# Kernel tuning notes

Hardware: AMD Instinct MI355X
Metric: run time of the kernel (lower is better)

## Reference

```python
import jax, jax.numpy as jnp
import numpy as np

B, V, H, T, D, HD = 4, 384, 128, 16, 8, 64
N = V + H  # 512
relu = jax.nn.relu


def setup_inputs() -> dict:
    key = jax.random.key(0)
    ks = jax.random.split(key, 12)

    def w(k, i, o):
        return (jax.random.normal(k, (i, o), jnp.float32) / np.sqrt(i)).astype(jnp.float32)

    return {
        "x": jax.random.normal(ks[0], (B, V, T, D), jnp.float32),
        "adj": jax.random.uniform(ks[1], (B, N, N), jnp.float32),
        # input_proj: Linear(T*D, HD) -> ReLU -> Linear(HD, HD) -> ReLU
        "w_in1": w(ks[2], T * D, HD), "b_in1": jnp.zeros((HD,), jnp.float32),
        "w_in2": w(ks[3], HD, HD), "b_in2": jnp.zeros((HD,), jnp.float32),
        # edge_mlp: Linear(2*HD, HD) -> ReLU -> Linear(HD, HD) -> ReLU
        "w_e1": w(ks[4], 2 * HD, HD), "b_e1": jnp.zeros((HD,), jnp.float32),
        "w_e2": w(ks[5], HD, HD), "b_e2": jnp.zeros((HD,), jnp.float32),
        # node_mlp: Linear(HD, HD) -> ReLU -> Linear(HD, HD) -> ReLU
        "w_n1": w(ks[6], HD, HD), "b_n1": jnp.zeros((HD,), jnp.float32),
        "w_n2": w(ks[7], HD, HD), "b_n2": jnp.zeros((HD,), jnp.float32),
        # out_proj: Linear(HD, T*D)
        "w_out": w(ks[8], HD, T * D), "b_out": jnp.zeros((T * D,), jnp.float32),
    }


def reference(x, adj, w_in1, b_in1, w_in2, b_in2, w_e1, b_e1, w_e2, b_e2,
              w_n1, b_n1, w_n2, b_n2, w_out, b_out):
    # node embedding of visible nodes: (B,V,HD)
    h = relu(relu(x.reshape(B, V, T * D) @ w_in1 + b_in1) @ w_in2 + b_in2)
    # pad hidden nodes with zeros: (B,N,HD)
    h_full = jnp.zeros((B, N, HD), x.dtype).at[:, :V].set(h)
    # edge_mlp layer 1 on cat([h_i, h_j]): split weight instead of materializing
    # the (B,N,N,2*HD) concatenation — same math.
    a = h_full @ w_e1[:HD]   # receiver-side contribution (B,N,HD)
    b = h_full @ w_e1[HD:]   # sender-side contribution  (B,N,HD)
    e = relu(a[:, :, None, :] + b[:, None, :, :] + b_e1)   # (B,N,N,HD)
    e = relu(e @ w_e2 + b_e2)                               # (B,N,N,HD)
    # mask by adjacency and sum over senders j
    agg = jnp.einsum('bijh,bij->bih', e, adj)               # (B,N,HD)
    n = relu(relu(agg @ w_n1 + b_n1) @ w_n2 + b_n2)         # (B,N,HD)
    out = n[:, V:] @ w_out + b_out                          # (B,H,T*D)
    return out.reshape(B, H, T, D)
```

## Files before the change

kernel.cpp:

```cpp
#include <hip/hip_runtime.h>

#define BQ 4
#define VV 384
#define HH 128
#define NN 512
#define HDIM 64
#define TD 128

typedef float f32x2 __attribute__((ext_vector_type(2)));

__device__ __forceinline__ float BCAST(float v, int l) {
    return __int_as_float(__builtin_amdgcn_readlane(__float_as_int(v), l));
}
__device__ __forceinline__ f32x2 RELU2(f32x2 v) {
    f32x2 r; r.x = fmaxf(v.x, 0.f); r.y = fmaxf(v.y, 0.f); return r;
}

__global__ __launch_bounds__(512) void k_rowpipe(
    const float* __restrict__ x,
    const float* __restrict__ w_in1,
    const float* __restrict__ b_in1,
    const float* __restrict__ w_in2,
    const float* __restrict__ b_in2,
    const float* __restrict__ w_e1,
    const float* __restrict__ b_e1,
    const float* __restrict__ w_e2,
    const float* __restrict__ b_e2,
    float* __restrict__ E2)
{
    __shared__ f32x2 part[4][8][HDIM];

    const int o    = threadIdx.x >> 6;
    const int lane = threadIdx.x & 63;
    const int row0 = blockIdx.x * 2;

    const float* xr0 = x + (size_t)row0 * TD;
    const float* xr1 = xr0 + TD;
    const float xv = (lane < 32) ? xr0[16 * o + (lane & 15)]
                                 : xr1[16 * o + (lane & 15)];

    f32x2 a0 = {0.f, 0.f}, a1 = {0.f, 0.f};
    #pragma unroll
    for (int k = 0; k < 16; k += 2) {
        const int kg = 16 * o + k;
        f32x2 s0; s0.x = BCAST(xv, k);     s0.y = BCAST(xv, 32 + k);
        f32x2 s1; s1.x = BCAST(xv, k + 1); s1.y = BCAST(xv, 33 + k);
        a0 += s0 * w_in1[kg * HDIM + lane];
        a1 += s1 * w_in1[(kg + 1) * HDIM + lane];
    }
    part[0][o][lane] = a0 + a1;
    __syncthreads();
    f32x2 t = ((part[0][0][lane] + part[0][1][lane])
             + (part[0][2][lane] + part[0][3][lane]))
            + ((part[0][4][lane] + part[0][5][lane])
             + (part[0][6][lane] + part[0][7][lane]));
    const f32x2 h1 = RELU2(t + b_in1[lane]);
    const float h1x = h1.x, h1y = h1.y;

    a0 = (f32x2){0.f, 0.f}; a1 = (f32x2){0.f, 0.f};
    #pragma unroll
    for (int k = 0; k < 8; k += 2) {
        const int kg = 8 * o + k;
        f32x2 s0; s0.x = BCAST(h1x, kg);     s0.y = BCAST(h1y, kg);
        f32x2 s1; s1.x = BCAST(h1x, kg + 1); s1.y = BCAST(h1y, kg + 1);
        a0 += s0 * w_in2[kg * HDIM + lane];
        a1 += s1 * w_in2[(kg + 1) * HDIM + lane];
    }
    part[1][o][lane] = a0 + a1;
    __syncthreads();
    t = ((part[1][0][lane] + part[1][1][lane])
       + (part[1][2][lane] + part[1][3][lane]))
      + ((part[1][4][lane] + part[1][5][lane])
       + (part[1][6][lane] + part[1][7][lane]));
    const f32x2 h2 = RELU2(t + b_in2[lane]);
    const float h2x = h2.x, h2y = h2.y;

    a0 = (f32x2){0.f, 0.f}; a1 = (f32x2){0.f, 0.f};
    #pragma unroll
    for (int k = 0; k < 8; k += 2) {
        const int kg = 8 * o + k;
        f32x2 s0; s0.x = BCAST(h2x, kg);     s0.y = BCAST(h2y, kg);
        f32x2 s1; s1.x = BCAST(h2x, kg + 1); s1.y = BCAST(h2y, kg + 1);
        a0 += s0 * w_e1[(HDIM + kg) * HDIM + lane];
        a1 += s1 * w_e1[(HDIM + kg + 1) * HDIM + lane];
    }
    part[2][o][lane] = a0 + a1;
    __syncthreads();
    t = ((part[2][0][lane] + part[2][1][lane])
       + (part[2][2][lane] + part[2][3][lane]))
      + ((part[2][4][lane] + part[2][5][lane])
       + (part[2][6][lane] + part[2][7][lane]));
    const f32x2 e1 = RELU2(t + b_e1[lane]);
    const float e1x = e1.x, e1y = e1.y;

    a0 = (f32x2){0.f, 0.f}; a1 = (f32x2){0.f, 0.f};
    #pragma unroll
    for (int k = 0; k < 8; k += 2) {
        const int kg = 8 * o + k;
        f32x2 s0; s0.x = BCAST(e1x, kg);     s0.y = BCAST(e1y, kg);
        f32x2 s1; s1.x = BCAST(e1x, kg + 1); s1.y = BCAST(e1y, kg + 1);
        a0 += s0 * w_e2[kg * HDIM + lane];
        a1 += s1 * w_e2[(kg + 1) * HDIM + lane];
    }
    part[3][o][lane] = a0 + a1;
    __syncthreads();
    if (o == 0) {
        t = ((part[3][0][lane] + part[3][1][lane])
           + (part[3][2][lane] + part[3][3][lane]))
          + ((part[3][4][lane] + part[3][5][lane])
           + (part[3][6][lane] + part[3][7][lane]));
        const f32x2 e2v = RELU2(t + b_e2[lane]);
        E2[(size_t)row0 * HDIM + lane]       = e2v.x;
        E2[(size_t)(row0 + 1) * HDIM + lane] = e2v.y;
    }
}

__global__ __launch_bounds__(1024) void k_agg_out(
    const float* __restrict__ adj,
    const float* __restrict__ E2,
    const float* __restrict__ b_e1, const float* __restrict__ w_e2,
    const float* __restrict__ b_e2,
    const float* __restrict__ w_n1, const float* __restrict__ b_n1,
    const float* __restrict__ w_n2, const float* __restrict__ b_n2,
    const float* __restrict__ w_out,
    const float* __restrict__ b_out,
    float* __restrict__ out)
{
    const int blk  = blockIdx.x;
    const int b    = blk >> 6;
    const int pair = blk & 63;
    const int wid  = threadIdx.x >> 6;
    const int lane = threadIdx.x & 63;

    const int i0 = VV + pair * 2;
    const float* adjr0 = adj + ((size_t)b * NN + i0) * NN;
    const float* adjr1 = adjr0 + NN;
    const int j0 = wid * 32;

    const float adjv = (lane < 32) ? adjr0[j0 + lane] : adjr1[j0 + lane - 32];

    __shared__ float redA[12][2][HDIM];
    __shared__ float hs[4][2];
    __shared__ float e2c[HDIM];

    if (wid < 12) {
        const float* e2b = E2 + ((size_t)b * VV + j0) * HDIM;
        float p0 = 0.f, p1 = 0.f, q0 = 0.f, q1 = 0.f;
        #pragma unroll 8
        for (int jj = 0; jj < 32; jj += 2) {
            const float e0 = e2b[jj * HDIM + lane];
            const float e1 = e2b[(jj + 1) * HDIM + lane];
            p0 = fmaf(BCAST(adjv, jj),      e0, p0);
            q0 = fmaf(BCAST(adjv, 32 + jj), e0, q0);
            p1 = fmaf(BCAST(adjv, jj + 1),  e1, p1);
            q1 = fmaf(BCAST(adjv, 33 + jj), e1, q1);
        }
        redA[wid][0][lane] = p0 + p1;
        redA[wid][1][lane] = q0 + q1;
    } else {
        float s = adjv;
        s += __shfl_xor(s, 1, 64);
        s += __shfl_xor(s, 2, 64);
        s += __shfl_xor(s, 4, 64);
        s += __shfl_xor(s, 8, 64);
        s += __shfl_xor(s, 16, 64);
        if (lane == 0)  hs[wid - 12][0] = s;
        if (lane == 32) hs[wid - 12][1] = s;
        if (wid == 12) {
            const float e1c = fmaxf(b_e1[lane], 0.f);
            float t0 = b_e2[lane], t1 = 0.f;
            #pragma unroll 8
            for (int k = 0; k < HDIM; k += 2) {
                t0 = fmaf(BCAST(e1c, k),     w_e2[k * HDIM + lane],       t0);
                t1 = fmaf(BCAST(e1c, k + 1), w_e2[(k + 1) * HDIM + lane], t1);
            }
            e2c[lane] = fmaxf(t0 + t1, 0.f);
        }
    }
    __syncthreads();

    const int g  = wid >> 3;
    const int w8 = wid & 7;

    const float hsum = hs[0][g] + hs[1][g] + hs[2][g] + hs[3][g];
    float agg = hsum * e2c[lane];
    #pragma unroll
    for (int w = 0; w < 12; ++w) agg += redA[w][g][lane];

    __shared__ float redB[16][HDIM];
    {
        float t0 = 0.f, t1 = 0.f;
        #pragma unroll
        for (int t = 0; t < 8; t += 2) {
            const int k = 8 * w8 + t;
            t0 = fmaf(BCAST(agg, k),     w_n1[k * HDIM + lane],       t0);
            t1 = fmaf(BCAST(agg, k + 1), w_n1[(k + 1) * HDIM + lane], t1);
        }
        redB[wid][lane] = t0 + t1;
    }
    __syncthreads();
    float n1 = b_n1[lane];
    #pragma unroll
    for (int w = 0; w < 8; ++w) n1 += redB[g * 8 + w][lane];
    n1 = fmaxf(n1, 0.f);

    __shared__ float redC[16][HDIM];
    {
        float t0 = 0.f, t1 = 0.f;
        #pragma unroll
        for (int t = 0; t < 8; t += 2) {
            const int k = 8 * w8 + t;
            t0 = fmaf(BCAST(n1, k),     w_n2[k * HDIM + lane],       t0);
            t1 = fmaf(BCAST(n1, k + 1), w_n2[(k + 1) * HDIM + lane], t1);
        }
        redC[wid][lane] = t0 + t1;
    }
    __syncthreads();
    float n2 = b_n2[lane];
    #pragma unroll
    for (int w = 0; w < 8; ++w) n2 += redC[g * 8 + w][lane];
    n2 = fmaxf(n2, 0.f);

    __shared__ float redD[16][TD];
    {
        float o0 = 0.f, o1 = 0.f;
        #pragma unroll
        for (int t = 0; t < 8; ++t) {
            const int k = 8 * w8 + t;
            const float v = BCAST(n2, k);
            o0 = fmaf(v, w_out[k * TD + lane],      o0);
            o1 = fmaf(v, w_out[k * TD + 64 + lane], o1);
        }
        redD[wid][lane]      = o0;
        redD[wid][64 + lane] = o1;
    }
    __syncthreads();

    if (w8 < 2) {
        const int col = w8 * 64 + lane;
        float o = b_out[col];
        #pragma unroll
        for (int w = 0; w < 8; ++w) o += redD[g * 8 + w][col];
        const int orow = b * HH + pair * 2 + g;
        out[(size_t)orow * TD + col] = o;
    }
}

extern "C" void kernel_launch(void* const* d_in, const int* in_sizes, int n_in,
                              void* d_out, int out_size, void* d_ws, size_t ws_size,
                              hipStream_t stream) {
    const float* x     = (const float*)d_in[0];
    const float* adj   = (const float*)d_in[1];
    const float* w_in1 = (const float*)d_in[2];
    const float* b_in1 = (const float*)d_in[3];
    const float* w_in2 = (const float*)d_in[4];
    const float* b_in2 = (const float*)d_in[5];
    const float* w_e1  = (const float*)d_in[6];
    const float* b_e1  = (const float*)d_in[7];
    const float* w_e2  = (const float*)d_in[8];
    const float* b_e2  = (const float*)d_in[9];
    const float* w_n1  = (const float*)d_in[10];
    const float* b_n1  = (const float*)d_in[11];
    const float* w_n2  = (const float*)d_in[12];
    const float* b_n2  = (const float*)d_in[13];
    const float* w_out = (const float*)d_in[14];
    const float* b_out = (const float*)d_in[15];
    float* out = (float*)d_out;
    float* E2  = (float*)d_ws;

    k_rowpipe<<<BQ * VV / 2, 512, 0, stream>>>(
        x, w_in1, b_in1, w_in2, b_in2, w_e1, b_e1, w_e2, b_e2, E2);
    k_agg_out<<<BQ * HH / 2, 1024, 0, stream>>>(
        adj, E2, b_e1, w_e2, b_e2, w_n1, b_n1, w_n2, b_n2, w_out, b_out, out);
}
```

Before: 16.04 us.

## Move hidden-sender adjacency sums and constant edge vector into first kernel

Adds a ninth wave to the row-pipeline kernel that computes, for each hidden receiver row, the adjacency sum over hidden senders, plus the constant edge-MLP output for zero-embedding nodes. Both are written to workspace. The aggregation kernel can then spread all 16 waves over the 384 visible senders (24 each) instead of keeping 4 waves mostly idle. This aims to cut the critical path of the second kernel. In exchange, the first kernel runs larger blocks whose extra wave just matches the __syncthreads calls, and the second kernel does extra global reads.

```diff
diff --git a/kernel.cpp b/kernel.cpp
--- a/kernel.cpp
+++ b/kernel.cpp
@@ -16,8 +16,13 @@
     f32x2 r; r.x = fmaxf(v.x, 0.f); r.y = fmaxf(v.y, 0.f); return r;
 }
 
-__global__ __launch_bounds__(512) void k_rowpipe(
+#define OFF_E2   0
+#define OFF_HSUM (BQ * VV * HDIM)
+#define OFF_E2C  (OFF_HSUM + BQ * HH)
+
+__global__ __launch_bounds__(576) void k_rowpipe(
     const float* __restrict__ x,
+    const float* __restrict__ adj,
     const float* __restrict__ w_in1,
     const float* __restrict__ b_in1,
     const float* __restrict__ w_in2,
@@ -26,12 +31,44 @@
     const float* __restrict__ b_e1,
     const float* __restrict__ w_e2,
     const float* __restrict__ b_e2,
-    float* __restrict__ E2)
+    float* __restrict__ E2,
+    float* __restrict__ hsumW,
+    float* __restrict__ e2cW)
 {
     __shared__ f32x2 part[4][8][HDIM];
 
-    const int o    = threadIdx.x >> 6;
+    const int wid  = threadIdx.x >> 6;
     const int lane = threadIdx.x & 63;
+
+    if (wid == 8) {
+        if (blockIdx.x < BQ * HH) {
+            const int hr = blockIdx.x;
+            const int b  = hr >> 7;
+            const int hi = hr & 127;
+            const float* ar = adj + ((size_t)b * NN + VV + hi) * NN + VV;
+            float s = ar[lane] + ar[64 + lane];
+            s += __shfl_xor(s, 32, 64);
+            s += __shfl_xor(s, 16, 64);
+            s += __shfl_xor(s, 8, 64);
+            s += __shfl_xor(s, 4, 64);
+            s += __shfl_xor(s, 2, 64);
+            s += __shfl_xor(s, 1, 64);
+            if (lane == 0) hsumW[hr] = s;
+        } else if (blockIdx.x == BQ * HH) {
+            const float e1c = fmaxf(b_e1[lane], 0.f);
+            float t0 = b_e2[lane], t1 = 0.f;
+            #pragma unroll 8
+            for (int k = 0; k < HDIM; k += 2) {
+                t0 = fmaf(BCAST(e1c, k),     w_e2[k * HDIM + lane],       t0);
+                t1 = fmaf(BCAST(e1c, k + 1), w_e2[(k + 1) * HDIM + lane], t1);
+            }
+            e2cW[lane] = fmaxf(t0 + t1, 0.f);
+        }
+        __syncthreads(); __syncthreads(); __syncthreads(); __syncthreads();
+        return;
+    }
+
+    const int o    = wid;
     const int row0 = blockIdx.x * 2;
 
     const float* xr0 = x + (size_t)row0 * TD;
@@ -118,8 +155,8 @@
 __global__ __launch_bounds__(1024) void k_agg_out(
     const float* __restrict__ adj,
     const float* __restrict__ E2,
-    const float* __restrict__ b_e1, const float* __restrict__ w_e2,
-    const float* __restrict__ b_e2,
+    const float* __restrict__ hsumW,
+    const float* __restrict__ e2cW,
     const float* __restrict__ w_n1, const float* __restrict__ b_n1,
     const float* __restrict__ w_n2, const float* __restrict__ b_n2,
     const float* __restrict__ w_out,
@@ -135,19 +172,17 @@
     const int i0 = VV + pair * 2;
     const float* adjr0 = adj + ((size_t)b * NN + i0) * NN;
     const float* adjr1 = adjr0 + NN;
-    const int j0 = wid * 32;
+    const int j0 = wid * 24;
 
     const float adjv = (lane < 32) ? adjr0[j0 + lane] : adjr1[j0 + lane - 32];
 
-    __shared__ float redA[12][2][HDIM];
-    __shared__ float hs[4][2];
-    __shared__ float e2c[HDIM];
-
-    if (wid < 12) {
+    __shared__ float redA[16][2][HDIM];
+
+    {
         const float* e2b = E2 + ((size_t)b * VV + j0) * HDIM;
         float p0 = 0.f, p1 = 0.f, q0 = 0.f, q1 = 0.f;
-        #pragma unroll 8
-        for (int jj = 0; jj < 32; jj += 2) {
+        #pragma unroll
+        for (int jj = 0; jj < 24; jj += 2) {
             const float e0 = e2b[jj * HDIM + lane];
             const float e1 = e2b[(jj + 1) * HDIM + lane];
             p0 = fmaf(BCAST(adjv, jj),      e0, p0);
@@ -157,35 +192,16 @@
         }
         redA[wid][0][lane] = p0 + p1;
         redA[wid][1][lane] = q0 + q1;
-    } else {
-        float s = adjv;
-        s += __shfl_xor(s, 1, 64);
-        s += __shfl_xor(s, 2, 64);
-        s += __shfl_xor(s, 4, 64);
-        s += __shfl_xor(s, 8, 64);
-        s += __shfl_xor(s, 16, 64);
-        if (lane == 0)  hs[wid - 12][0] = s;
-        if (lane == 32) hs[wid - 12][1] = s;
-        if (wid == 12) {
-            const float e1c = fmaxf(b_e1[lane], 0.f);
-            float t0 = b_e2[lane], t1 = 0.f;
-            #pragma unroll 8
-            for (int k = 0; k < HDIM; k += 2) {
-                t0 = fmaf(BCAST(e1c, k),     w_e2[k * HDIM + lane],       t0);
-                t1 = fmaf(BCAST(e1c, k + 1), w_e2[(k + 1) * HDIM + lane], t1);
-            }
-            e2c[lane] = fmaxf(t0 + t1, 0.f);
-        }
     }
     __syncthreads();
 
     const int g  = wid >> 3;
     const int w8 = wid & 7;
 
-    const float hsum = hs[0][g] + hs[1][g] + hs[2][g] + hs[3][g];
-    float agg = hsum * e2c[lane];
-    #pragma unroll
-    for (int w = 0; w < 12; ++w) agg += redA[w][g][lane];
+    const float hsum = hsumW[b * HH + pair * 2 + g];
+    float agg = hsum * e2cW[lane];
+    #pragma unroll
+    for (int w = 0; w < 16; ++w) agg += redA[w][g][lane];
 
     __shared__ float redB[16][HDIM];
     {
@@ -265,11 +281,15 @@
     const float* b_n2  = (const float*)d_in[13];
     const float* w_out = (const float*)d_in[14];
     const float* b_out = (const float*)d_in[15];
-    float* out = (float*)d_out;
-    float* E2  = (float*)d_ws;
-
-    k_rowpipe<<<BQ * VV / 2, 512, 0, stream>>>(
-        x, w_in1, b_in1, w_in2, b_in2, w_e1, b_e1, w_e2, b_e2, E2);
+    float* out   = (float*)d_out;
+    float* ws    = (float*)d_ws;
+    float* E2    = ws + OFF_E2;
+    float* hsumW = ws + OFF_HSUM;
+    float* e2cW  = ws + OFF_E2C;
+
+    k_rowpipe<<<BQ * VV / 2, 576, 0, stream>>>(
+        x, adj, w_in1, b_in1, w_in2, b_in2, w_e1, b_e1, w_e2, b_e2,
+        E2, hsumW, e2cW);
     k_agg_out<<<BQ * HH / 2, 1024, 0, stream>>>(
-        adj, E2, b_e1, w_e2, b_e2, w_n1, b_n1, w_n2, b_n2, w_out, b_out, out);
-}
+        adj, E2, hsumW, e2cW, w_n1, b_n1, w_n2, b_n2, w_out, b_out, out);
+}
```

Result: slower. 16.43 us (+2.4%).

## Split aggregation to one row per block and precompute hidden-sender term

Applied to the files above, without the earlier changes.

The aggregation kernel moves from two output rows per block (256 blocks) to one row per block (512 blocks). Each of the 16 waves now sums 24 visible senders, and one extra wave also sums the adjacency weights of the hidden senders. The constant edge output for hidden senders, already passed through w_n1, is now computed once in the first block of the row kernel and stored in the workspace. The node MLP then adds it as a scaled bias, which removes that work from every aggregation block. The cost is more blocks that each reload E2 and the weights, and half the waves sit idle during the MLP stages.

```diff
diff --git a/kernel.cpp b/kernel.cpp
--- a/kernel.cpp
+++ b/kernel.cpp
@@ -15,6 +15,9 @@
 __device__ __forceinline__ f32x2 RELU2(f32x2 v) {
     f32x2 r; r.x = fmaxf(v.x, 0.f); r.y = fmaxf(v.y, 0.f); return r;
 }
+
+#define OFF_E2 0
+#define OFF_C1 (BQ * VV * HDIM)
 
 __global__ __launch_bounds__(512) void k_rowpipe(
     const float* __restrict__ x,
@@ -26,7 +29,9 @@
     const float* __restrict__ b_e1,
     const float* __restrict__ w_e2,
     const float* __restrict__ b_e2,
-    float* __restrict__ E2)
+    const float* __restrict__ w_n1,
+    float* __restrict__ E2,
+    float* __restrict__ c1W)
 {
     __shared__ f32x2 part[4][8][HDIM];
 
@@ -112,104 +117,102 @@
         const f32x2 e2v = RELU2(t + b_e2[lane]);
         E2[(size_t)row0 * HDIM + lane]       = e2v.x;
         E2[(size_t)(row0 + 1) * HDIM + lane] = e2v.y;
+    } else if (o == 1 && blockIdx.x == 0) {
+        const float e1c = fmaxf(b_e1[lane], 0.f);
+        float t0 = b_e2[lane], t1 = 0.f;
+        #pragma unroll 8
+        for (int k = 0; k < HDIM; k += 2) {
+            t0 = fmaf(BCAST(e1c, k),     w_e2[k * HDIM + lane],       t0);
+            t1 = fmaf(BCAST(e1c, k + 1), w_e2[(k + 1) * HDIM + lane], t1);
+        }
+        const float e2c = fmaxf(t0 + t1, 0.f);
+        t0 = 0.f; t1 = 0.f;
+        #pragma unroll 8
+        for (int k = 0; k < HDIM; k += 2) {
+            t0 = fmaf(BCAST(e2c, k),     w_n1[k * HDIM + lane],       t0);
+            t1 = fmaf(BCAST(e2c, k + 1), w_n1[(k + 1) * HDIM + lane], t1);
+        }
+        c1W[lane] = t0 + t1;
     }
 }
 
 __global__ __launch_bounds__(1024) void k_agg_out(
     const float* __restrict__ adj,
     const float* __restrict__ E2,
-    const float* __restrict__ b_e1, const float* __restrict__ w_e2,
-    const float* __restrict__ b_e2,
+    const float* __restrict__ c1W,
     const float* __restrict__ w_n1, const float* __restrict__ b_n1,
     const float* __restrict__ w_n2, const float* __restrict__ b_n2,
     const float* __restrict__ w_out,
     const float* __restrict__ b_out,
     float* __restrict__ out)
 {
-    const int blk  = blockIdx.x;
-    const int b    = blk >> 6;
-    const int pair = blk & 63;
+    const int row  = blockIdx.x;
+    const int b    = row >> 7;
+    const int hi   = row & 127;
+    const int i    = VV + hi;
     const int wid  = threadIdx.x >> 6;
     const int lane = threadIdx.x & 63;
 
-    const int i0 = VV + pair * 2;
-    const float* adjr0 = adj + ((size_t)b * NN + i0) * NN;
-    const float* adjr1 = adjr0 + NN;
-    const int j0 = wid * 32;
-
-    const float adjv = (lane < 32) ? adjr0[j0 + lane] : adjr1[j0 + lane - 32];
-
-    __shared__ float redA[12][2][HDIM];
-    __shared__ float hs[4][2];
-    __shared__ float e2c[HDIM];
-
-    if (wid < 12) {
+    const float* adjrow = adj + ((size_t)b * NN + i) * NN;
+    const int j0 = wid * 24;
+
+    const float adjv = adjrow[j0 + lane];
+
+    __shared__ float redA[16][HDIM];
+    __shared__ float hsLDS;
+
+    {
         const float* e2b = E2 + ((size_t)b * VV + j0) * HDIM;
-        float p0 = 0.f, p1 = 0.f, q0 = 0.f, q1 = 0.f;
-        #pragma unroll 8
-        for (int jj = 0; jj < 32; jj += 2) {
+        float p0 = 0.f, p1 = 0.f;
+        #pragma unroll
+        for (int jj = 0; jj < 24; jj += 2) {
             const float e0 = e2b[jj * HDIM + lane];
             const float e1 = e2b[(jj + 1) * HDIM + lane];
-            p0 = fmaf(BCAST(adjv, jj),      e0, p0);
-            q0 = fmaf(BCAST(adjv, 32 + jj), e0, q0);
-            p1 = fmaf(BCAST(adjv, jj + 1),  e1, p1);
-            q1 = fmaf(BCAST(adjv, 33 + jj), e1, q1);
-        }
-        redA[wid][0][lane] = p0 + p1;
-        redA[wid][1][lane] = q0 + q1;
-    } else {
-        float s = adjv;
+            p0 = fmaf(BCAST(adjv, jj),     e0, p0);
+            p1 = fmaf(BCAST(adjv, jj + 1), e1, p1);
+        }
+        redA[wid][lane] = p0 + p1;
+    }
+    if (wid == 15) {
+        float s = adjrow[VV + lane] + adjrow[VV + 64 + lane];
+        s += __shfl_xor(s, 32, 64);
+        s += __shfl_xor(s, 16, 64);
+        s += __shfl_xor(s, 8, 64);
+        s += __shfl_xor(s, 4, 64);
+        s += __shfl_xor(s, 2, 64);
         s += __shfl_xor(s, 1, 64);
-        s += __shfl_xor(s, 2, 64);
-        s += __shfl_xor(s, 4, 64);
-        s += __shfl_xor(s, 8, 64);
-        s += __shfl_xor(s, 16, 64);
-        if (lane == 0)  hs[wid - 12][0] = s;
-        if (lane == 32) hs[wid - 12][1] = s;
-        if (wid == 12) {
-            const float e1c = fmaxf(b_e1[lane], 0.f);
-            float t0 = b_e2[lane], t1 = 0.f;
-            #pragma unroll 8
-            for (int k = 0; k < HDIM; k += 2) {
-                t0 = fmaf(BCAST(e1c, k),     w_e2[k * HDIM + lane],       t0);
-                t1 = fmaf(BCAST(e1c, k + 1), w_e2[(k + 1) * HDIM + lane], t1);
-            }
-            e2c[lane] = fmaxf(t0 + t1, 0.f);
-        }
-    }
-    __syncthreads();
-
-    const int g  = wid >> 3;
-    const int w8 = wid & 7;
-
-    const float hsum = hs[0][g] + hs[1][g] + hs[2][g] + hs[3][g];
-    float agg = hsum * e2c[lane];
-    #pragma unroll
-    for (int w = 0; w < 12; ++w) agg += redA[w][g][lane];
-
-    __shared__ float redB[16][HDIM];
-    {
+        if (lane == 0) hsLDS = s;
+    }
+    __syncthreads();
+
+    float agg = 0.f;
+    #pragma unroll
+    for (int w = 0; w < 16; ++w) agg += redA[w][lane];
+    const float hsum = hsLDS;
+
+    __shared__ float redB[8][HDIM];
+    if (wid < 8) {
         float t0 = 0.f, t1 = 0.f;
         #pragma unroll
         for (int t = 0; t < 8; t += 2) {
-            const int k = 8 * w8 + t;
+            const int k = 8 * wid + t;
             t0 = fmaf(BCAST(agg, k),     w_n1[k * HDIM + lane],       t0);
             t1 = fmaf(BCAST(agg, k + 1), w_n1[(k + 1) * HDIM + lane], t1);
         }
         redB[wid][lane] = t0 + t1;
     }
     __syncthreads();
-    float n1 = b_n1[lane];
-    #pragma unroll
-    for (int w = 0; w < 8; ++w) n1 += redB[g * 8 + w][lane];
+    float n1 = fmaf(hsum, c1W[lane], b_n1[lane]);
+    #pragma unroll
+    for (int w = 0; w < 8; ++w) n1 += redB[w][lane];
     n1 = fmaxf(n1, 0.f);
 
-    __shared__ float redC[16][HDIM];
-    {
+    __shared__ float redC[8][HDIM];
+    if (wid < 8) {
         float t0 = 0.f, t1 = 0.f;
         #pragma unroll
         for (int t = 0; t < 8; t += 2) {
-            const int k = 8 * w8 + t;
+            const int k = 8 * wid + t;
             t0 = fmaf(BCAST(n1, k),     w_n2[k * HDIM + lane],       t0);
             t1 = fmaf(BCAST(n1, k + 1), w_n2[(k + 1) * HDIM + lane], t1);
         }
@@ -218,15 +221,15 @@
     __syncthreads();
     float n2 = b_n2[lane];
     #pragma unroll
-    for (int w = 0; w < 8; ++w) n2 += redC[g * 8 + w][lane];
+    for (int w = 0; w < 8; ++w) n2 += redC[w][lane];
     n2 = fmaxf(n2, 0.f);
 
-    __shared__ float redD[16][TD];
-    {
+    __shared__ float redD[8][TD];
+    if (wid < 8) {
         float o0 = 0.f, o1 = 0.f;
         #pragma unroll
         for (int t = 0; t < 8; ++t) {
-            const int k = 8 * w8 + t;
+            const int k = 8 * wid + t;
             const float v = BCAST(n2, k);
             o0 = fmaf(v, w_out[k * TD + lane],      o0);
             o1 = fmaf(v, w_out[k * TD + 64 + lane], o1);
@@ -236,13 +239,12 @@
     }
     __syncthreads();
 
-    if (w8 < 2) {
-        const int col = w8 * 64 + lane;
+    if (wid < 2) {
+        const int col = wid * 64 + lane;
         float o = b_out[col];
         #pragma unroll
-        for (int w = 0; w < 8; ++w) o += redD[g * 8 + w][col];
-        const int orow = b * HH + pair * 2 + g;
-        out[(size_t)orow * TD + col] = o;
+        for (int w = 0; w < 8; ++w) o += redD[w][col];
+        out[(size_t)row * TD + col] = o;
     }
 }
 
@@ -265,11 +267,13 @@
     const float* b_n2  = (const float*)d_in[13];
     const float* w_out = (const float*)d_in[14];
     const float* b_out = (const float*)d_in[15];
-    float* out = (float*)d_out;
-    float* E2  = (float*)d_ws;
+    float* out  = (float*)d_out;
+    float* ws   = (float*)d_ws;
+    float* E2   = ws + OFF_E2;
+    float* c1W  = ws + OFF_C1;
 
     k_rowpipe<<<BQ * VV / 2, 512, 0, stream>>>(
-        x, w_in1, b_in1, w_in2, b_in2, w_e1, b_e1, w_e2, b_e2, E2);
-    k_agg_out<<<BQ * HH / 2, 1024, 0, stream>>>(
-        adj, E2, b_e1, w_e2, b_e2, w_n1, b_n1, w_n2, b_n2, w_out, b_out, out);
-}
+        x, w_in1, b_in1, w_in2, b_in2, w_e1, b_e1, w_e2, b_e2, w_n1, E2, c1W);
+    k_agg_out<<<BQ * HH, 1024, 0, stream>>>(
+        adj, E2, c1W, w_n1, b_n1, w_n2, b_n2, w_out, b_out, out);
+}
```

After: 16.52 us. +2.9%, slower.
